# Optimization experiments

Hardware: AMD Instinct MI355X
Metric: run time of the kernel (lower is better)

Reference implementation:

```python
import jax, jax.numpy as jnp
import numpy as np

DT = 0.1
THRESH = 10.0

def setup_inputs() -> dict:
    key = jax.random.key(0)
    ks = jax.random.split(key, 6)
    B, S, H, V = 2, 1024, 1024, 50257
    hidden_states = jax.random.normal(ks[0], (B, S, H), dtype=jnp.float32)
    ttu_state = jnp.zeros((B, 3), dtype=jnp.float32)
    W_imp = jax.random.normal(ks[1], (3, H), dtype=jnp.float32) * 0.02
    b_imp = jnp.zeros((3,), dtype=jnp.float32)
    W_lm = jax.random.normal(ks[2], (V, H), dtype=jnp.float32) * 0.02
    W_mod = jax.random.normal(ks[3], (V, 3), dtype=jnp.float32) * 0.02
    # gamma, alpha_c, beta_c, delta, alpha_d, epsilon, alpha_m
    ttu_params = jax.random.uniform(ks[4], (7,), dtype=jnp.float32, minval=0.1, maxval=1.0)
    return {"hidden_states": hidden_states, "ttu_state": ttu_state,
            "W_imp": W_imp, "b_imp": b_imp, "W_lm": W_lm, "W_mod": W_mod,
            "ttu_params": ttu_params}

def _ttu_scan(ttu_state, impulses, ttu_params):
    # impulses: [S, B, 3] (time-major for scan)
    gamma, alpha_c, beta_c, delta, alpha_d, epsilon, alpha_m = ttu_params
    def step(state, imp):
        phi_c, phi_d, phi_m = state[:, 0], state[:, 1], state[:, 2]
        dphi_c = gamma * imp[:, 0] - alpha_c * phi_c - beta_c * phi_c * phi_d
        dphi_d = delta * phi_c ** 2 - alpha_d * phi_d
        dphi_m = epsilon * phi_d - alpha_m * phi_m
        new_c = phi_c + DT * dphi_c
        new_d = phi_d + DT * dphi_d
        new_m = phi_m + DT * dphi_m
        # saturation damping on phi_d
        new_d = jnp.where(jnp.abs(new_d) > THRESH, jnp.float32(0.5), jnp.float32(1.0)) * new_d
        new_state = jnp.stack([new_c, new_d, new_m], axis=1)  # [B, 3]
        return new_state, new_state
    return jax.lax.scan(step, ttu_state, impulses)

def reference(hidden_states, ttu_state, W_imp, b_imp, W_lm, W_mod, ttu_params):
    # impulse projections computed in batch up front: [S, B, 3]
    impulses = jnp.einsum('bsh,dh->sbd', hidden_states, W_imp) + b_imp
    final_state, states = _ttu_scan(ttu_state, impulses, ttu_params)  # states: [S, B, 3]
    # base lm logits + 0.1 * modulation from ttu trajectory
    logits = jnp.einsum('bsh,vh->bsv', hidden_states, W_lm) \
           + 0.1 * jnp.einsum('sbd,vd->bsv', states, W_mod)
    return logits, final_state
```

## Files before the change

kernel.cpp:

```cpp
#include <hip/hip_runtime.h>
#include <hip/hip_bf16.h>

typedef float  f32x4  __attribute__((ext_vector_type(4)));
typedef short  bf16x8 __attribute__((ext_vector_type(8)));
typedef short  bf16x4 __attribute__((ext_vector_type(4)));

typedef const void __attribute__((address_space(1))) gv_t;
typedef void __attribute__((address_space(3))) sv_t;

namespace {

constexpr int B_ = 2;
constexpr int S_ = 1024;
constexpr int H_ = 1024;
constexpr int V_ = 50257;
constexpr int M_ = B_ * S_;
constexpr int VP2_ = 50432;
constexpr int VP1_ = 50304;
constexpr float DT_ = 0.1f;
constexpr float THRESH_ = 10.0f;

constexpr int BK = 64;
constexpr int NT = H_ / BK;

__device__ __forceinline__ unsigned short f2bf(float f) {
  union { float f; unsigned u; } x;
  x.f = f;
  x.u += 0x7FFFu + ((x.u >> 16) & 1u);
  return (unsigned short)(x.u >> 16);
}

__global__ void cvt_hidden_impulse_kernel(const float* __restrict__ hidden,
                                          const float* __restrict__ W_imp,
                                          const float* __restrict__ b_imp,
                                          unsigned short* __restrict__ hid_bf,
                                          float* __restrict__ imp) {
  const int m = blockIdx.x;
  const int t = threadIdx.x;
  const float4 hv = reinterpret_cast<const float4*>(hidden + (size_t)m * H_)[t];
  const float4 wv = reinterpret_cast<const float4*>(W_imp)[t];
  bf16x4 o;
  o[0] = (short)f2bf(hv.x); o[1] = (short)f2bf(hv.y);
  o[2] = (short)f2bf(hv.z); o[3] = (short)f2bf(hv.w);
  *(bf16x4*)(hid_bf + (size_t)m * H_ + t * 4) = o;
  float p = hv.x * wv.x + hv.y * wv.y + hv.z * wv.z + hv.w * wv.w;
  #pragma unroll
  for (int off = 32; off; off >>= 1) p += __shfl_down(p, off);
  __shared__ float partial[4];
  if ((t & 63) == 0) partial[t >> 6] = p;
  __syncthreads();
  if (t == 0) {
    const float v = partial[0] + partial[1] + partial[2] + partial[3] + b_imp[0];
    const int b = m >> 10;
    const int s = m & (S_ - 1);
    imp[s * B_ + b] = v;
  }
}

__device__ __forceinline__ void scan_body(const float* __restrict__ imp_s,
                                          const float* __restrict__ ttu_state,
                                          const float* __restrict__ ttu_params,
                                          float* __restrict__ states,
                                          float* __restrict__ final_out, int t) {
  if (t < B_) {
    const float gamma   = ttu_params[0];
    const float alpha_c = ttu_params[1];
    const float beta_c  = ttu_params[2];
    const float delta   = ttu_params[3];
    const float alpha_d = ttu_params[4];
    const float epsilon = ttu_params[5];
    const float alpha_m = ttu_params[6];
    float c = ttu_state[t * 3 + 0];
    float d = ttu_state[t * 3 + 1];
    float m = ttu_state[t * 3 + 2];
    for (int s = 0; s < S_; ++s) {
      const float ii = imp_s[s * B_ + t];
      const float dc = gamma * ii - alpha_c * c - beta_c * c * d;
      const float dd = delta * c * c - alpha_d * d;
      const float dm = epsilon * d - alpha_m * m;
      c = c + DT_ * dc;
      float nd = d + DT_ * dd;
      m = m + DT_ * dm;
      nd = (fabsf(nd) > THRESH_ ? 0.5f : 1.0f) * nd;
      d = nd;
      float* st = states + (size_t)(s * B_ + t) * 3;
      st[0] = c; st[1] = d; st[2] = m;
    }
    final_out[t * 3 + 0] = c;
    final_out[t * 3 + 1] = d;
    final_out[t * 3 + 2] = m;
  }
}

__global__ void ttu_scan_kernel(const float* __restrict__ imp,
                                const float* __restrict__ ttu_state,
                                const float* __restrict__ ttu_params,
                                float* __restrict__ states,
                                float* __restrict__ final_out) {
  __shared__ float imp_s[S_ * B_];
  const int t = threadIdx.x;
  for (int i = t; i < S_ * B_; i += 64) imp_s[i] = imp[i];
  __syncthreads();
  scan_body(imp_s, ttu_state, ttu_params, states, final_out, t);
}

__global__ void cvt_wlm_scan_kernel(const float* __restrict__ src,
                                    unsigned short* __restrict__ dst,
                                    long n_src, long n_dst,
                                    const float* __restrict__ imp,
                                    const float* __restrict__ ttu_state,
                                    const float* __restrict__ ttu_params,
                                    float* __restrict__ states,
                                    float* __restrict__ final_out) {
  __shared__ float imp_s[S_ * B_];
  const int t = threadIdx.x;
  if (blockIdx.x == gridDim.x - 1) {
    for (int i = t; i < S_ * B_; i += 256) imp_s[i] = imp[i];
    __syncthreads();
    scan_body(imp_s, ttu_state, ttu_params, states, final_out, t);
    return;
  }
  const long stride = (long)(gridDim.x - 1) * blockDim.x * 8;
  for (long i = ((long)blockIdx.x * blockDim.x + t) * 8; i < n_dst; i += stride) {
    bf16x8 v;
    if (i < n_src) {
      const float4 a = *(const float4*)(src + i);
      const float4 b = *(const float4*)(src + i + 4);
      v[0] = (short)f2bf(a.x); v[1] = (short)f2bf(a.y);
      v[2] = (short)f2bf(a.z); v[3] = (short)f2bf(a.w);
      v[4] = (short)f2bf(b.x); v[5] = (short)f2bf(b.y);
      v[6] = (short)f2bf(b.z); v[7] = (short)f2bf(b.w);
    } else {
      v = (bf16x8){0, 0, 0, 0, 0, 0, 0, 0};
    }
    *(bf16x8*)(dst + i) = v;
  }
}

__global__ void cvt_bf16_kernel(const float* __restrict__ src,
                                unsigned short* __restrict__ dst,
                                long n_src, long n_dst) {
  const long stride = (long)gridDim.x * blockDim.x * 8;
  for (long i = ((long)blockIdx.x * blockDim.x + threadIdx.x) * 8; i < n_dst; i += stride) {
    bf16x8 v;
    if (i < n_src) {
      const float4 a = *(const float4*)(src + i);
      const float4 b = *(const float4*)(src + i + 4);
      v[0] = (short)f2bf(a.x); v[1] = (short)f2bf(a.y);
      v[2] = (short)f2bf(a.z); v[3] = (short)f2bf(a.w);
      v[4] = (short)f2bf(b.x); v[5] = (short)f2bf(b.y);
      v[6] = (short)f2bf(b.z); v[7] = (short)f2bf(b.w);
    } else {
      v = (bf16x8){0, 0, 0, 0, 0, 0, 0, 0};
    }
    *(bf16x8*)(dst + i) = v;
  }
}

__global__ __launch_bounds__(512, 2) void ttu_gemm_bf16_256_kernel(
    const unsigned short* __restrict__ Ab,
    const unsigned short* __restrict__ Bb,
    const float* __restrict__ states,
    const float* __restrict__ Wmod,
    float* __restrict__ out)
{
  __shared__ unsigned short A_s[2][256 * BK];
  __shared__ unsigned short B_s[2][256 * BK];
  __shared__ float st_s[256][3];
  __shared__ float wm_s[256][3];

  const int t = threadIdx.x;
  const int cpx = gridDim.x >> 3;
  const int bid = (blockIdx.x & 7) * cpx + (blockIdx.x >> 3);
  const int mb = bid & 7;
  const int nb = bid >> 3;
  const int m0 = mb * 256;
  const int n0 = nb * 256;

  if (t < 256) {
    const int m = m0 + t;
    const int b = m >> 10;
    const int s = m & (S_ - 1);
    const float* st = states + (size_t)(s * B_ + b) * 3;
    st_s[t][0] = st[0]; st_s[t][1] = st[1]; st_s[t][2] = st[2];
  } else {
    const int tt = t - 256;
    const int n = n0 + tt;
    const bool ok = n < V_;
    wm_s[tt][0] = ok ? Wmod[n * 3 + 0] : 0.f;
    wm_s[tt][1] = ok ? Wmod[n * 3 + 1] : 0.f;
    wm_s[tt][2] = ok ? Wmod[n * 3 + 2] : 0.f;
  }

  const int lane = t & 63;
  const int wid  = t >> 6;
  const int lr   = lane >> 3;
  const int ch   = lane & 7;
  const int wmi  = wid >> 2;
  const int wni  = wid & 3;
  const int lm   = lane & 15;
  const int kg   = lane >> 4;

  const unsigned short* Abase = Ab + (size_t)m0 * H_;
  const unsigned short* Bbase = Bb + (size_t)n0 * H_;

  auto STAGE_HALF = [&](int buf, int kt, int h) {
    const int k0 = kt * BK;
    const unsigned short* gb = (h < 2) ? Abase : Bbase;
    unsigned short* ls = (h < 2) ? &A_s[buf][0] : &B_s[buf][0];
    const int half = (h & 1) * 128;
    #pragma unroll
    for (int n = 0; n < 2; ++n) {
      const int rbase = half + wid * 16 + n * 8;
      const int r  = rbase + lr;
      const int sc = ch ^ (r & 7);
      __builtin_amdgcn_global_load_lds(
          (gv_t*)(gb + (size_t)r * H_ + k0 + sc * 8),
          (sv_t*)(ls + rbase * BK), 16, 0, 0);
    }
  };

  f32x4 acc[8][4];
  #pragma unroll
  for (int i = 0; i < 8; ++i)
    #pragma unroll
    for (int j = 0; j < 4; ++j)
      acc[i][j] = (f32x4){0.f, 0.f, 0.f, 0.f};

  #pragma unroll
  for (int h = 0; h < 4; ++h) STAGE_HALF(0, 0, h);
  asm volatile("s_waitcnt vmcnt(0)" ::: "memory");
  __builtin_amdgcn_s_barrier();
  __builtin_amdgcn_sched_barrier(0);

  int cur = 0;
  bf16x8 bfr[4][2];

  for (int kt = 0; kt < NT; ++kt) {
    const int nxt = cur ^ 1;
    const bool more = (kt + 1 < NT);
    const unsigned short* As = &A_s[cur][0];
    const unsigned short* Bs = &B_s[cur][0];

    if (more) {
      STAGE_HALF(nxt, kt + 1, 0);
      asm volatile("s_waitcnt vmcnt(2)" ::: "memory");
    } else {
      asm volatile("s_waitcnt vmcnt(0)" ::: "memory");
    }
    __builtin_amdgcn_s_barrier();
    __builtin_amdgcn_sched_barrier(0);

    #pragma unroll
    for (int q = 0; q < 4; ++q) {
      if (q > 0 && more) STAGE_HALF(nxt, kt + 1, q);
      if (q == 0) {
        #pragma unroll
        for (int j = 0; j < 4; ++j)
          #pragma unroll
          for (int ks = 0; ks < 2; ++ks) {
            const int r = wni * 64 + j * 16 + lm;
            bfr[j][ks] = *(const bf16x8*)&Bs[r * BK + (((ks * 4 + kg) ^ (r & 7)) << 3)];
          }
      }
      bf16x8 af[2][2];
      #pragma unroll
      for (int i2 = 0; i2 < 2; ++i2)
        #pragma unroll
        for (int ks = 0; ks < 2; ++ks) {
          const int r = wmi * 128 + (q * 2 + i2) * 16 + lm;
          af[i2][ks] = *(const bf16x8*)&As[r * BK + (((ks * 4 + kg) ^ (r & 7)) << 3)];
        }
      asm volatile("s_waitcnt lgkmcnt(0)" ::: "memory");
      __builtin_amdgcn_sched_barrier(0);
      __builtin_amdgcn_s_setprio(1);
      #pragma unroll
      for (int ks = 0; ks < 2; ++ks)
        #pragma unroll
        for (int i2 = 0; i2 < 2; ++i2)
          #pragma unroll
          for (int j = 0; j < 4; ++j)
            acc[q * 2 + i2][j] = __builtin_amdgcn_mfma_f32_16x16x32_bf16(
                af[i2][ks], bfr[j][ks], acc[q * 2 + i2][j], 0, 0, 0);
      __builtin_amdgcn_s_setprio(0);
    }

    __builtin_amdgcn_s_barrier();
    __builtin_amdgcn_sched_barrier(0);
    cur ^= 1;
  }

  #pragma unroll
  for (int i = 0; i < 8; ++i) {
    #pragma unroll
    for (int rr = 0; rr < 4; ++rr) {
      const int mloc = wmi * 128 + i * 16 + kg * 4 + rr;
      const float s0 = st_s[mloc][0], s1 = st_s[mloc][1], s2 = st_s[mloc][2];
      float* orow = out + (size_t)(m0 + mloc) * V_ + n0;
      #pragma unroll
      for (int j = 0; j < 4; ++j) {
        const int nloc = wni * 64 + j * 16 + lm;
        if (n0 + nloc < V_) {
          const float corr = 0.1f * (s0 * wm_s[nloc][0] + s1 * wm_s[nloc][1] + s2 * wm_s[nloc][2]);
          orow[nloc] = acc[i][j][rr] + corr;
        }
      }
    }
  }
}

__global__ __launch_bounds__(256) void ttu_gemm_bf16_db_kernel(
    const unsigned short* __restrict__ Ab,
    const unsigned short* __restrict__ Bb,
    const float* __restrict__ states,
    const float* __restrict__ Wmod,
    float* __restrict__ out)
{
  __shared__ unsigned short AB_s[2][2][128 * BK];
  __shared__ float st_s[128][3];
  __shared__ float wm_s[128][3];

  const int t = threadIdx.x;
  const int cpx = gridDim.x >> 3;
  const int bid = (blockIdx.x & 7) * cpx + (blockIdx.x >> 3);
  const int mb = bid & 15;
  const int nb = bid >> 4;
  const int m0 = mb * 128;
  const int n0 = nb * 128;

  if (t < 128) {
    const int m = m0 + t;
    const int b = m >> 10;
    const int s = m & (S_ - 1);
    const float* st = states + (size_t)(s * B_ + b) * 3;
    st_s[t][0] = st[0]; st_s[t][1] = st[1]; st_s[t][2] = st[2];
  } else {
    const int tt = t - 128;
    const int n = n0 + tt;
    const bool ok = n < V_;
    wm_s[tt][0] = ok ? Wmod[n * 3 + 0] : 0.f;
    wm_s[tt][1] = ok ? Wmod[n * 3 + 1] : 0.f;
    wm_s[tt][2] = ok ? Wmod[n * 3 + 2] : 0.f;
  }

  const int lane = t & 63;
  const int wid  = t >> 6;
  const int lr   = lane >> 3;
  const int ch   = lane & 7;
  const int wm   = wid >> 1;
  const int wn   = wid & 1;
  const int lm   = lane & 15;
  const int kg   = lane >> 4;

  const unsigned short* Abase = Ab + (size_t)m0 * H_;
  const unsigned short* Bbase = Bb + (size_t)n0 * H_;
  const int r0 = wid * 32;

  auto STAGE = [&](unsigned short* As, unsigned short* Bs, int kt) {
    const int k0 = kt * BK;
    #pragma unroll
    for (int ins = 0; ins < 4; ++ins) {
      const int lrow = r0 + ins * 8 + lr;
      const int sch  = ch ^ (lrow & 7);
      __builtin_amdgcn_global_load_lds(
          (gv_t*)(Abase + (size_t)lrow * H_ + k0 + sch * 8),
          (sv_t*)(As + (r0 + ins * 8) * BK), 16, 0, 0);
    }
    #pragma unroll
    for (int ins = 0; ins < 4; ++ins) {
      const int lrow = r0 + ins * 8 + lr;
      const int sch  = ch ^ (lrow & 7);
      __builtin_amdgcn_global_load_lds(
          (gv_t*)(Bbase + (size_t)lrow * H_ + k0 + sch * 8),
          (sv_t*)(Bs + (r0 + ins * 8) * BK), 16, 0, 0);
    }
  };

  f32x4 acc[4][4];
  #pragma unroll
  for (int i = 0; i < 4; ++i)
    #pragma unroll
    for (int j = 0; j < 4; ++j)
      acc[i][j] = (f32x4){0.f, 0.f, 0.f, 0.f};

  unsigned short* Ac = &AB_s[0][0][0];
  unsigned short* Bc = &AB_s[0][1][0];
  unsigned short* An = &AB_s[1][0][0];
  unsigned short* Bn = &AB_s[1][1][0];

  STAGE(Ac, Bc, 0);
  __syncthreads();

  for (int kt = 0; kt < NT; ++kt) {
    if (kt + 1 < NT) STAGE(An, Bn, kt + 1);
    bf16x8 af[4][2], bfr[4][2];
    #pragma unroll
    for (int i = 0; i < 4; ++i) {
      const int arow = wm * 64 + i * 16 + lm;
      const int brow = wn * 64 + i * 16 + lm;
      #pragma unroll
      for (int ks = 0; ks < 2; ++ks) {
        af[i][ks]  = *(const bf16x8*)&Ac[arow * BK + (((ks * 4 + kg) ^ (arow & 7)) << 3)];
        bfr[i][ks] = *(const bf16x8*)&Bc[brow * BK + (((ks * 4 + kg) ^ (brow & 7)) << 3)];
      }
    }
    #pragma unroll
    for (int ks = 0; ks < 2; ++ks)
      #pragma unroll
      for (int i = 0; i < 4; ++i)
        #pragma unroll
        for (int j = 0; j < 4; ++j)
          acc[i][j] = __builtin_amdgcn_mfma_f32_16x16x32_bf16(af[i][ks], bfr[j][ks], acc[i][j], 0, 0, 0);
    __syncthreads();
    unsigned short* tp;
    tp = Ac; Ac = An; An = tp;
    tp = Bc; Bc = Bn; Bn = tp;
  }

  #pragma unroll
  for (int i = 0; i < 4; ++i) {
    #pragma unroll
    for (int rr = 0; rr < 4; ++rr) {
      const int mloc = wm * 64 + i * 16 + kg * 4 + rr;
      const float s0 = st_s[mloc][0], s1 = st_s[mloc][1], s2 = st_s[mloc][2];
      float* orow = out + (size_t)(m0 + mloc) * V_ + n0;
      #pragma unroll
      for (int j = 0; j < 4; ++j) {
        const int nloc = wn * 64 + j * 16 + lm;
        if (n0 + nloc < V_) {
          const float corr = 0.1f * (s0 * wm_s[nloc][0] + s1 * wm_s[nloc][1] + s2 * wm_s[nloc][2]);
          orow[nloc] = acc[i][j][rr] + corr;
        }
      }
    }
  }
}

__global__ __launch_bounds__(256) void ttu_gemm_kernel(
    const float* __restrict__ Ag, const float* __restrict__ Bg,
    const float* __restrict__ states, const float* __restrict__ Wmod,
    float* __restrict__ out)
{
  __shared__ unsigned short A_s[128][40];
  __shared__ unsigned short B_s[128][40];
  __shared__ float st_s[128][3];
  __shared__ float wm_s[128][3];

  const int t   = threadIdx.x;
  const int bid = blockIdx.x;
  const int mb  = bid & 15;
  const int nb  = bid >> 4;
  const int m0  = mb * 128;
  const int n0  = nb * 128;

  if (t < 128) {
    const int m = m0 + t;
    const int b = m >> 10;
    const int s = m & (S_ - 1);
    const float* st = states + (size_t)(s * B_ + b) * 3;
    st_s[t][0] = st[0]; st_s[t][1] = st[1]; st_s[t][2] = st[2];
  } else {
    const int tt = t - 128;
    const int n  = n0 + tt;
    const bool ok = n < V_;
    wm_s[tt][0] = ok ? Wmod[n * 3 + 0] : 0.f;
    wm_s[tt][1] = ok ? Wmod[n * 3 + 1] : 0.f;
    wm_s[tt][2] = ok ? Wmod[n * 3 + 2] : 0.f;
  }

  const int r   = t >> 1;
  const int seg = t & 1;
  const float* arow = Ag + (size_t)(m0 + r) * H_ + seg * 16;
  const int  vrow = n0 + r;
  const bool bok  = vrow < V_;
  const float* brow = Bg + (size_t)(bok ? vrow : 0) * H_ + seg * 16;

  const int lane = t & 63;
  const int wid  = t >> 6;
  const int wm   = wid >> 1;
  const int wn   = wid & 1;
  const int lm   = lane & 15;
  const int kg   = lane >> 4;

  f32x4 acc[4][4];
  #pragma unroll
  for (int i = 0; i < 4; ++i)
    #pragma unroll
    for (int j = 0; j < 4; ++j)
      acc[i][j] = (f32x4){0.f, 0.f, 0.f, 0.f};

  for (int kt = 0; kt < H_ / 32; ++kt) {
    const int k0 = kt * 32;
    const float4 av0 = *(const float4*)(arow + k0 + 0);
    const float4 av1 = *(const float4*)(arow + k0 + 4);
    const float4 av2 = *(const float4*)(arow + k0 + 8);
    const float4 av3 = *(const float4*)(arow + k0 + 12);
    float4 bv0 = {0,0,0,0}, bv1 = {0,0,0,0}, bv2 = {0,0,0,0}, bv3 = {0,0,0,0};
    if (bok) {
      bv0 = *(const float4*)(brow + k0 + 0);
      bv1 = *(const float4*)(brow + k0 + 4);
      bv2 = *(const float4*)(brow + k0 + 8);
      bv3 = *(const float4*)(brow + k0 + 12);
    }
    __syncthreads();
    #define CVT4(v) (bf16x4){(short)f2bf((v).x), (short)f2bf((v).y), (short)f2bf((v).z), (short)f2bf((v).w)}
    *(bf16x4*)&A_s[r][seg * 16 + 0]  = CVT4(av0);
    *(bf16x4*)&A_s[r][seg * 16 + 4]  = CVT4(av1);
    *(bf16x4*)&A_s[r][seg * 16 + 8]  = CVT4(av2);
    *(bf16x4*)&A_s[r][seg * 16 + 12] = CVT4(av3);
    *(bf16x4*)&B_s[r][seg * 16 + 0]  = CVT4(bv0);
    *(bf16x4*)&B_s[r][seg * 16 + 4]  = CVT4(bv1);
    *(bf16x4*)&B_s[r][seg * 16 + 8]  = CVT4(bv2);
    *(bf16x4*)&B_s[r][seg * 16 + 12] = CVT4(bv3);
    #undef CVT4
    __syncthreads();
    bf16x8 af[4], bf[4];
    #pragma unroll
    for (int i = 0; i < 4; ++i) {
      af[i] = *(const bf16x8*)&A_s[wm * 64 + i * 16 + lm][kg * 8];
      bf[i] = *(const bf16x8*)&B_s[wn * 64 + i * 16 + lm][kg * 8];
    }
    #pragma unroll
    for (int i = 0; i < 4; ++i)
      #pragma unroll
      for (int j = 0; j < 4; ++j)
        acc[i][j] = __builtin_amdgcn_mfma_f32_16x16x32_bf16(af[i], bf[j], acc[i][j], 0, 0, 0);
  }

  #pragma unroll
  for (int i = 0; i < 4; ++i) {
    #pragma unroll
    for (int rr = 0; rr < 4; ++rr) {
      const int mloc = wm * 64 + i * 16 + kg * 4 + rr;
      const float s0 = st_s[mloc][0], s1 = st_s[mloc][1], s2 = st_s[mloc][2];
      float* orow = out + (size_t)(m0 + mloc) * V_ + n0;
      #pragma unroll
      for (int j = 0; j < 4; ++j) {
        const int nloc = wn * 64 + j * 16 + lm;
        if (n0 + nloc < V_) {
          const float corr = 0.1f * (s0 * wm_s[nloc][0] + s1 * wm_s[nloc][1] + s2 * wm_s[nloc][2]);
          orow[nloc] = acc[i][j][rr] + corr;
        }
      }
    }
  }
}

}

extern "C" void kernel_launch(void* const* d_in, const int* in_sizes, int n_in,
                              void* d_out, int out_size, void* d_ws, size_t ws_size,
                              hipStream_t stream) {
  const float* hidden     = (const float*)d_in[0];
  const float* ttu_state  = (const float*)d_in[1];
  const float* W_imp      = (const float*)d_in[2];
  const float* b_imp      = (const float*)d_in[3];
  const float* W_lm       = (const float*)d_in[4];
  const float* W_mod      = (const float*)d_in[5];
  const float* ttu_params = (const float*)d_in[6];
  float* out = (float*)d_out;

  float* imp    = (float*)d_ws;
  float* states = imp + S_ * B_;
  float* final_out = out + (size_t)B_ * S_ * V_;

  const size_t need256 = 32768 + (size_t)M_ * H_ * 2 + (size_t)VP2_ * H_ * 2;
  const size_t need128 = 32768 + (size_t)M_ * H_ * 2 + (size_t)VP1_ * H_ * 2;

  if (ws_size >= need256) {
    unsigned short* hid_bf = (unsigned short*)((char*)d_ws + 32768);
    unsigned short* wlm_bf = hid_bf + (size_t)M_ * H_;
    cvt_hidden_impulse_kernel<<<M_, 256, 0, stream>>>(hidden, W_imp, b_imp, hid_bf, imp);
    cvt_wlm_scan_kernel<<<4097, 256, 0, stream>>>(W_lm, wlm_bf,
                                                  (long)V_ * H_, (long)VP2_ * H_,
                                                  imp, ttu_state, ttu_params,
                                                  states, final_out);
    const int grid = (VP2_ / 256) * (M_ / 256);
    ttu_gemm_bf16_256_kernel<<<grid, 512, 0, stream>>>(hid_bf, wlm_bf, states, W_mod, out);
  } else if (ws_size >= need128) {
    unsigned short* hid_bf = (unsigned short*)((char*)d_ws + 32768);
    unsigned short* wlm_bf = hid_bf + (size_t)M_ * H_;
    cvt_hidden_impulse_kernel<<<M_, 256, 0, stream>>>(hidden, W_imp, b_imp, hid_bf, imp);
    ttu_scan_kernel<<<1, 64, 0, stream>>>(imp, ttu_state, ttu_params, states, final_out);
    cvt_bf16_kernel<<<4096, 256, 0, stream>>>(W_lm, wlm_bf, (long)V_ * H_, (long)VP1_ * H_);
    const int grid = (VP1_ / 128) * (M_ / 128);
    ttu_gemm_bf16_db_kernel<<<grid, 256, 0, stream>>>(hid_bf, wlm_bf, states, W_mod, out);
  } else {
    cvt_hidden_impulse_kernel<<<M_, 256, 0, stream>>>(hidden, W_imp, b_imp,
                                                      (unsigned short*)d_ws, imp);
    ttu_scan_kernel<<<1, 64, 0, stream>>>(imp, ttu_state, ttu_params, states, final_out);
    const int grid = ((V_ + 127) / 128) * (M_ / 128);
    ttu_gemm_kernel<<<grid, 256, 0, stream>>>(hidden, W_lm, states, W_mod, out);
  }
}
```

Before: 550.8 us.

## Issue all next-tile loads up front and double-buffer A fragments in registers

```diff
diff --git a/kernel.cpp b/kernel.cpp
--- a/kernel.cpp
+++ b/kernel.cpp
@@ -157,7 +157,7 @@
   }
 }
 
-__global__ __launch_bounds__(512, 2) void ttu_gemm_bf16_256_kernel(
+__global__ __launch_bounds__(512, 2) void ttu_gemm_bf16_256v2_kernel(
     const unsigned short* __restrict__ Ab,
     const unsigned short* __restrict__ Bb,
     const float* __restrict__ states,
@@ -204,19 +204,22 @@
   const unsigned short* Abase = Ab + (size_t)m0 * H_;
   const unsigned short* Bbase = Bb + (size_t)n0 * H_;
 
-  auto STAGE_HALF = [&](int buf, int kt, int h) {
+  auto STAGE_ALL = [&](int buf, int kt) {
     const int k0 = kt * BK;
-    const unsigned short* gb = (h < 2) ? Abase : Bbase;
-    unsigned short* ls = (h < 2) ? &A_s[buf][0] : &B_s[buf][0];
-    const int half = (h & 1) * 128;
-    #pragma unroll
-    for (int n = 0; n < 2; ++n) {
-      const int rbase = half + wid * 16 + n * 8;
-      const int r  = rbase + lr;
-      const int sc = ch ^ (r & 7);
-      __builtin_amdgcn_global_load_lds(
-          (gv_t*)(gb + (size_t)r * H_ + k0 + sc * 8),
-          (sv_t*)(ls + rbase * BK), 16, 0, 0);
+    #pragma unroll
+    for (int h = 0; h < 4; ++h) {
+      const unsigned short* gb = (h < 2) ? Abase : Bbase;
+      unsigned short* ls = (h < 2) ? &A_s[buf][0] : &B_s[buf][0];
+      const int half = (h & 1) * 128;
+      #pragma unroll
+      for (int n = 0; n < 2; ++n) {
+        const int rbase = half + wid * 16 + n * 8;
+        const int r  = rbase + lr;
+        const int sc = ch ^ (r & 7);
+        __builtin_amdgcn_global_load_lds(
+            (gv_t*)(gb + (size_t)r * H_ + k0 + sc * 8),
+            (sv_t*)(ls + rbase * BK), 16, 0, 0);
+      }
     }
   };
 
@@ -227,52 +230,51 @@
     for (int j = 0; j < 4; ++j)
       acc[i][j] = (f32x4){0.f, 0.f, 0.f, 0.f};
 
-  #pragma unroll
-  for (int h = 0; h < 4; ++h) STAGE_HALF(0, 0, h);
-  asm volatile("s_waitcnt vmcnt(0)" ::: "memory");
-  __builtin_amdgcn_s_barrier();
-  __builtin_amdgcn_sched_barrier(0);
+  STAGE_ALL(0, 0);
 
   int cur = 0;
-  bf16x8 bfr[4][2];
-
   for (int kt = 0; kt < NT; ++kt) {
     const int nxt = cur ^ 1;
-    const bool more = (kt + 1 < NT);
+    asm volatile("s_barrier" ::: "memory");
+    if (kt + 1 < NT) {
+      STAGE_ALL(nxt, kt + 1);
+      asm volatile("s_waitcnt vmcnt(8)" ::: "memory");
+    } else {
+      asm volatile("s_waitcnt vmcnt(0)" ::: "memory");
+    }
+    asm volatile("s_barrier" ::: "memory");
+
     const unsigned short* As = &A_s[cur][0];
     const unsigned short* Bs = &B_s[cur][0];
 
-    if (more) {
-      STAGE_HALF(nxt, kt + 1, 0);
-      asm volatile("s_waitcnt vmcnt(2)" ::: "memory");
-    } else {
-      asm volatile("s_waitcnt vmcnt(0)" ::: "memory");
-    }
-    __builtin_amdgcn_s_barrier();
-    __builtin_amdgcn_sched_barrier(0);
-
+    bf16x8 bfr[4][2];
+    #pragma unroll
+    for (int j = 0; j < 4; ++j)
+      #pragma unroll
+      for (int ks = 0; ks < 2; ++ks) {
+        const int r = wni * 64 + j * 16 + lm;
+        bfr[j][ks] = *(const bf16x8*)&Bs[r * BK + (((ks * 4 + kg) ^ (r & 7)) << 3)];
+      }
+    bf16x8 af[2][2][2];
+    #pragma unroll
+    for (int i2 = 0; i2 < 2; ++i2)
+      #pragma unroll
+      for (int ks = 0; ks < 2; ++ks) {
+        const int r = wmi * 128 + i2 * 16 + lm;
+        af[0][i2][ks] = *(const bf16x8*)&As[r * BK + (((ks * 4 + kg) ^ (r & 7)) << 3)];
+      }
     #pragma unroll
     for (int q = 0; q < 4; ++q) {
-      if (q > 0 && more) STAGE_HALF(nxt, kt + 1, q);
-      if (q == 0) {
+      if (q < 3) {
         #pragma unroll
-        for (int j = 0; j < 4; ++j)
+        for (int i2 = 0; i2 < 2; ++i2)
           #pragma unroll
           for (int ks = 0; ks < 2; ++ks) {
-            const int r = wni * 64 + j * 16 + lm;
-            bfr[j][ks] = *(const bf16x8*)&Bs[r * BK + (((ks * 4 + kg) ^ (r & 7)) << 3)];
+            const int r = wmi * 128 + ((q + 1) * 2 + i2) * 16 + lm;
+            af[(q + 1) & 1][i2][ks] =
+                *(const bf16x8*)&As[r * BK + (((ks * 4 + kg) ^ (r & 7)) << 3)];
           }
       }
-      bf16x8 af[2][2];
-      #pragma unroll
-      for (int i2 = 0; i2 < 2; ++i2)
-        #pragma unroll
-        for (int ks = 0; ks < 2; ++ks) {
-          const int r = wmi * 128 + (q * 2 + i2) * 16 + lm;
-          af[i2][ks] = *(const bf16x8*)&As[r * BK + (((ks * 4 + kg) ^ (r & 7)) << 3)];
-        }
-      asm volatile("s_waitcnt lgkmcnt(0)" ::: "memory");
-      __builtin_amdgcn_sched_barrier(0);
       __builtin_amdgcn_s_setprio(1);
       #pragma unroll
       for (int ks = 0; ks < 2; ++ks)
@@ -281,12 +283,9 @@
           #pragma unroll
           for (int j = 0; j < 4; ++j)
             acc[q * 2 + i2][j] = __builtin_amdgcn_mfma_f32_16x16x32_bf16(
-                af[i2][ks], bfr[j][ks], acc[q * 2 + i2][j], 0, 0, 0);
+                af[q & 1][i2][ks], bfr[j][ks], acc[q * 2 + i2][j], 0, 0, 0);
       __builtin_amdgcn_s_setprio(0);
     }
-
-    __builtin_amdgcn_s_barrier();
-    __builtin_amdgcn_sched_barrier(0);
     cur ^= 1;
   }
 
@@ -576,7 +575,7 @@
                                                   imp, ttu_state, ttu_params,
                                                   states, final_out);
     const int grid = (VP2_ / 256) * (M_ / 256);
-    ttu_gemm_bf16_256_kernel<<<grid, 512, 0, stream>>>(hid_bf, wlm_bf, states, W_mod, out);
+    ttu_gemm_bf16_256v2_kernel<<<grid, 512, 0, stream>>>(hid_bf, wlm_bf, states, W_mod, out);
   } else if (ws_size >= need128) {
     unsigned short* hid_bf = (unsigned short*)((char*)d_ws + 32768);
     unsigned short* wlm_bf = hid_bf + (size_t)M_ * H_;
```

Measured after the change: 483.6 us, median of 2. -12.2%, faster.

## Restructure 256x256 bf16 GEMM main loop into finer-grained software pipeline

Applied to the files above, without the earlier changes.

```diff
diff --git a/kernel.cpp b/kernel.cpp
--- a/kernel.cpp
+++ b/kernel.cpp
@@ -157,7 +157,12 @@
   }
 }
 
-__global__ __launch_bounds__(512, 2) void ttu_gemm_bf16_256_kernel(
+#define VMCNT(N) asm volatile("s_waitcnt vmcnt(" #N ")" ::: "memory")
+#define LGK(N)   asm volatile("s_waitcnt lgkmcnt(" #N ")" ::: "memory")
+#define BAR()    asm volatile("s_barrier" ::: "memory")
+#define SB0()    __builtin_amdgcn_sched_barrier(0)
+
+__global__ __launch_bounds__(512, 2) void ttu_gemm_bf16_256p4_kernel(
     const unsigned short* __restrict__ Ab,
     const unsigned short* __restrict__ Bb,
     const float* __restrict__ states,
@@ -204,21 +209,86 @@
   const unsigned short* Abase = Ab + (size_t)m0 * H_;
   const unsigned short* Bbase = Bb + (size_t)n0 * H_;
 
-  auto STAGE_HALF = [&](int buf, int kt, int h) {
-    const int k0 = kt * BK;
-    const unsigned short* gb = (h < 2) ? Abase : Bbase;
-    unsigned short* ls = (h < 2) ? &A_s[buf][0] : &B_s[buf][0];
-    const int half = (h & 1) * 128;
+  size_t bgo[2][2]; int bro[2][2];
+  size_t ago[2][2]; int aro[2][2];
+  #pragma unroll
+  for (int h = 0; h < 2; ++h)
     #pragma unroll
     for (int n = 0; n < 2; ++n) {
-      const int rbase = half + wid * 16 + n * 8;
-      const int r  = rbase + lr;
-      const int sc = ch ^ (r & 7);
-      __builtin_amdgcn_global_load_lds(
-          (gv_t*)(gb + (size_t)r * H_ + k0 + sc * 8),
-          (sv_t*)(ls + rbase * BK), 16, 0, 0);
-    }
-  };
+      const int rb = h * 128 + wid * 16 + n * 8;
+      const int r  = rb + lr;
+      bro[h][n] = rb * BK;
+      bgo[h][n] = (size_t)r * H_ + ((ch ^ (r & 7)) << 3);
+    }
+  #pragma unroll
+  for (int g = 0; g < 2; ++g)
+    #pragma unroll
+    for (int n = 0; n < 2; ++n) {
+      const int ib = wid * 16 + n * 8;
+      const int rb = g * 64 + (ib & 63) + ((ib >> 6) << 7);
+      const int r  = rb + lr;
+      aro[g][n] = rb * BK;
+      ago[g][n] = (size_t)r * H_ + ((ch ^ (r & 7)) << 3);
+    }
+
+#define STG_B(BUF, H, K0) do {                                                 \
+    __builtin_amdgcn_global_load_lds((gv_t*)(Bbase + bgo[H][0] + (K0)),        \
+                                     (sv_t*)((BUF) + bro[H][0]), 16, 0, 0);    \
+    __builtin_amdgcn_global_load_lds((gv_t*)(Bbase + bgo[H][1] + (K0)),        \
+                                     (sv_t*)((BUF) + bro[H][1]), 16, 0, 0);    \
+  } while (0)
+#define STG_A(BUF, G, K0) do {                                                 \
+    __builtin_amdgcn_global_load_lds((gv_t*)(Abase + ago[G][0] + (K0)),        \
+                                     (sv_t*)((BUF) + aro[G][0]), 16, 0, 0);    \
+    __builtin_amdgcn_global_load_lds((gv_t*)(Abase + ago[G][1] + (K0)),        \
+                                     (sv_t*)((BUF) + aro[G][1]), 16, 0, 0);    \
+  } while (0)
+#define RD_AQ(AS, Q) do {                                                      \
+    _Pragma("unroll") for (int i2_ = 0; i2_ < 2; ++i2_) {                      \
+      const int r_ = wmi * 128 + ((Q) * 2 + i2_) * 16 + lm;                    \
+      _Pragma("unroll") for (int ks_ = 0; ks_ < 2; ++ks_)                      \
+        af[i2_][ks_] = *(const bf16x8*)&(AS)[r_ * BK +                         \
+                        (((ks_ * 4 + kg) ^ (r_ & 7)) << 3)];                   \
+    }                                                                          \
+  } while (0)
+#define RD_BF(BF, BS) do {                                                     \
+    _Pragma("unroll") for (int j_ = 0; j_ < 4; ++j_) {                         \
+      const int r_ = wni * 64 + j_ * 16 + lm;                                  \
+      _Pragma("unroll") for (int ks_ = 0; ks_ < 2; ++ks_)                      \
+        BF[j_][ks_] = *(const bf16x8*)&(BS)[r_ * BK +                          \
+                       (((ks_ * 4 + kg) ^ (r_ & 7)) << 3)];                    \
+    }                                                                          \
+  } while (0)
+#define MFMA_Q(Q, BF) do {                                                     \
+    __builtin_amdgcn_s_setprio(1);                                             \
+    _Pragma("unroll") for (int ks_ = 0; ks_ < 2; ++ks_)                        \
+      _Pragma("unroll") for (int i2_ = 0; i2_ < 2; ++i2_)                      \
+        _Pragma("unroll") for (int j_ = 0; j_ < 4; ++j_)                       \
+          acc[(Q) * 2 + i2_][j_] = __builtin_amdgcn_mfma_f32_16x16x32_bf16(    \
+              af[i2_][ks_], BF[j_][ks_], acc[(Q) * 2 + i2_][j_], 0, 0, 0);     \
+    __builtin_amdgcn_s_setprio(0);                                             \
+  } while (0)
+#define DO_TILE(KT, AS, BS, ASN, BSN, BFC, BFN, ISLAST) do {                   \
+    const int k0n_ = ((KT) + 1) * BK;                                          \
+                                                                       \
+    RD_AQ(AS, 0);                                                              \
+    if (!(ISLAST)) { STG_B(BSN, 0, k0n_); VMCNT(2); } else { VMCNT(0); }       \
+    BAR(); LGK(0); SB0(); MFMA_Q(0, BFC); BAR();                               \
+                                                                       \
+    RD_AQ(AS, 1);                                                              \
+    if (!(ISLAST)) { STG_B(BSN, 1, k0n_); }                                    \
+    BAR(); LGK(0); SB0(); MFMA_Q(1, BFC); BAR();                               \
+                                                                       \
+    RD_AQ(AS, 2);                                                              \
+    if (!(ISLAST)) { STG_A(ASN, 0, k0n_); VMCNT(2); }                          \
+    BAR(); LGK(0); SB0(); MFMA_Q(2, BFC); BAR();                               \
+                                                                       \
+    RD_AQ(AS, 3);                                                              \
+    if (!(ISLAST)) { STG_A(ASN, 1, k0n_); VMCNT(2); }                          \
+    BAR();                                                                     \
+    if (!(ISLAST)) { RD_BF(BFN, BSN); LGK(8); } else { LGK(0); }               \
+    SB0(); MFMA_Q(3, BFC); BAR();                                              \
+  } while (0)
 
   f32x4 acc[8][4];
   #pragma unroll
@@ -227,67 +297,21 @@
     for (int j = 0; j < 4; ++j)
       acc[i][j] = (f32x4){0.f, 0.f, 0.f, 0.f};
 
-  #pragma unroll
-  for (int h = 0; h < 4; ++h) STAGE_HALF(0, 0, h);
-  asm volatile("s_waitcnt vmcnt(0)" ::: "memory");
-  __builtin_amdgcn_s_barrier();
-  __builtin_amdgcn_sched_barrier(0);
-
-  int cur = 0;
-  bf16x8 bfr[4][2];
-
-  for (int kt = 0; kt < NT; ++kt) {
-    const int nxt = cur ^ 1;
-    const bool more = (kt + 1 < NT);
-    const unsigned short* As = &A_s[cur][0];
-    const unsigned short* Bs = &B_s[cur][0];
-
-    if (more) {
-      STAGE_HALF(nxt, kt + 1, 0);
-      asm volatile("s_waitcnt vmcnt(2)" ::: "memory");
-    } else {
-      asm volatile("s_waitcnt vmcnt(0)" ::: "memory");
-    }
-    __builtin_amdgcn_s_barrier();
-    __builtin_amdgcn_sched_barrier(0);
-
-    #pragma unroll
-    for (int q = 0; q < 4; ++q) {
-      if (q > 0 && more) STAGE_HALF(nxt, kt + 1, q);
-      if (q == 0) {
-        #pragma unroll
-        for (int j = 0; j < 4; ++j)
-          #pragma unroll
-          for (int ks = 0; ks < 2; ++ks) {
-            const int r = wni * 64 + j * 16 + lm;
-            bfr[j][ks] = *(const bf16x8*)&Bs[r * BK + (((ks * 4 + kg) ^ (r & 7)) << 3)];
-          }
-      }
-      bf16x8 af[2][2];
-      #pragma unroll
-      for (int i2 = 0; i2 < 2; ++i2)
-        #pragma unroll
-        for (int ks = 0; ks < 2; ++ks) {
-          const int r = wmi * 128 + (q * 2 + i2) * 16 + lm;
-          af[i2][ks] = *(const bf16x8*)&As[r * BK + (((ks * 4 + kg) ^ (r & 7)) << 3)];
-        }
-      asm volatile("s_waitcnt lgkmcnt(0)" ::: "memory");
-      __builtin_amdgcn_sched_barrier(0);
-      __builtin_amdgcn_s_setprio(1);
-      #pragma unroll
-      for (int ks = 0; ks < 2; ++ks)
-        #pragma unroll
-        for (int i2 = 0; i2 < 2; ++i2)
-          #pragma unroll
-          for (int j = 0; j < 4; ++j)
-            acc[q * 2 + i2][j] = __builtin_amdgcn_mfma_f32_16x16x32_bf16(
-                af[i2][ks], bfr[j][ks], acc[q * 2 + i2][j], 0, 0, 0);
-      __builtin_amdgcn_s_setprio(0);
-    }
-
-    __builtin_amdgcn_s_barrier();
-    __builtin_amdgcn_sched_barrier(0);
-    cur ^= 1;
+  bf16x8 bfA[4][2], bfB[4][2], af[2][2];
+
+  STG_B(&B_s[0][0], 0, 0);
+  STG_B(&B_s[0][0], 1, 0);
+  STG_A(&A_s[0][0], 0, 0);
+  STG_A(&A_s[0][0], 1, 0);
+  VMCNT(2);
+  BAR();
+  RD_BF(bfA, &B_s[0][0]);
+
+  #pragma unroll 1
+  for (int ktp = 0; ktp < NT / 2; ++ktp) {
+    const int kt = ktp * 2;
+    DO_TILE(kt,     &A_s[0][0], &B_s[0][0], &A_s[1][0], &B_s[1][0], bfA, bfB, false);
+    DO_TILE(kt + 1, &A_s[1][0], &B_s[1][0], &A_s[0][0], &B_s[0][0], bfB, bfA, ktp == NT / 2 - 1);
   }
 
   #pragma unroll
@@ -307,6 +331,12 @@
       }
     }
   }
+#undef STG_B
+#undef STG_A
+#undef RD_AQ
+#undef RD_BF
+#undef MFMA_Q
+#undef DO_TILE
 }
 
 __global__ __launch_bounds__(256) void ttu_gemm_bf16_db_kernel(
@@ -571,12 +601,12 @@
     unsigned short* hid_bf = (unsigned short*)((char*)d_ws + 32768);
     unsigned short* wlm_bf = hid_bf + (size_t)M_ * H_;
     cvt_hidden_impulse_kernel<<<M_, 256, 0, stream>>>(hidden, W_imp, b_imp, hid_bf, imp);
-    cvt_wlm_scan_kernel<<<4097, 256, 0, stream>>>(W_lm, wlm_bf,
+    cvt_wlm_scan_kernel<<<2049, 256, 0, stream>>>(W_lm, wlm_bf,
                                                   (long)V_ * H_, (long)VP2_ * H_,
                                                   imp, ttu_state, ttu_params,
                                                   states, final_out);
     const int grid = (VP2_ / 256) * (M_ / 256);
-    ttu_gemm_bf16_256_kernel<<<grid, 512, 0, stream>>>(hid_bf, wlm_bf, states, W_mod, out);
+    ttu_gemm_bf16_256p4_kernel<<<grid, 512, 0, stream>>>(hid_bf, wlm_bf, states, W_mod, out);
   } else if (ws_size >= need128) {
     unsigned short* hid_bf = (unsigned short*)((char*)d_ws + 32768);
     unsigned short* wlm_bf = hid_bf + (size_t)M_ * H_;
```

New measurement: 600.0 us. +8.9%, slower.
